# Kernel optimization log

Measured on AMD Instinct MI355X. Metric: run time of the kernel, lower is better.

## Reference

```python
import jax, jax.numpy as jnp
import numpy as np

IN_FEATURES = 4096
OUT_FEATURES = 8192
PADDED = 8192  # 2**ceil(log2(out_features))


def fwht(x):
    """Fast Walsh-Hadamard transform over last axis (n power of 2), normalized by 1/sqrt(n)."""
    orig_shape = x.shape
    n = orig_shape[-1]
    h = x.reshape(-1, n)
    step = 1
    while step < n:  # static loop, log2(n) iterations
        h = h.reshape(-1, n // (2 * step), 2, step)
        a = h[:, :, 0, :]
        b = h[:, :, 1, :]
        h = jnp.stack([a + b, a - b], axis=2).reshape(-1, n)
        step *= 2
    return (h * (1.0 / np.sqrt(n)).astype(np.float32)).reshape(orig_shape)


def setup_inputs() -> dict:
    key = jax.random.key(0)
    kx, kb, kg, kp = jax.random.split(key, 4)
    x = jax.random.normal(kx, (8192, IN_FEATURES), dtype=jnp.float32)
    B = jnp.where(jax.random.uniform(kb, (PADDED,)) < 0.5, -1.0, 1.0).astype(jnp.float32)
    G = jax.random.normal(kg, (PADDED,), dtype=jnp.float32)
    perm = jax.random.permutation(kp, PADDED).astype(jnp.int32)
    return {"x": x, "B": B, "G": G, "perm": perm}


def reference(x, B, G, perm):
    lead = x.shape[:-1]
    flat = x.reshape(-1, IN_FEATURES)
    pad_len = PADDED - IN_FEATURES
    if pad_len > 0:
        flat = jnp.pad(flat, ((0, 0), (0, pad_len)))
    out = flat * B[None, :]
    out = fwht(out)
    out = out[:, perm]
    out = out * G[None, :]
    out = fwht(out)
    out = out[:, :OUT_FEATURES]
    return out.reshape(*lead, OUT_FEATURES)
```

## Files before the change

### kernel.cpp

```cpp
#include <hip/hip_runtime.h>


constexpr int N  = 8192;
constexpr int NT = 256;
constexpr int NR = 32;
constexpr int LDS_WORDS = N + 2 * (N / 32);

__device__ __forceinline__ int padw(int w) { return w + 2 * (w >> 5); }

template <int FIRST_MASK>
__device__ __forceinline__ void butterfly(float v[NR]) {
    #pragma unroll
    for (int b = FIRST_MASK; b < NR; b <<= 1) {
        #pragma unroll
        for (int r = 0; r < NR; ++r) {
            if ((r & b) == 0) {
                float a = v[r], c = v[r ^ b];
                v[r]     = a + c;
                v[r ^ b] = a - c;
            }
        }
    }
}

__global__ __launch_bounds__(NT, 4) void fastfood_kernel(
    const float* __restrict__ x, const float* __restrict__ Bv,
    const float* __restrict__ Gv, const int* __restrict__ perm,
    float* __restrict__ out)
{
    __shared__ float lds[LDS_WORDS];
    const int t = threadIdx.x;
    const int row = blockIdx.x;
    const float* xrow = x + (size_t)row * 4096;

    const int wA = 2 * t;
    const int wB = t * 32;
    const int wC = (t >> 4) * 512 + (t & 15) * 2;

    float v[NR];

    #pragma unroll
    for (int m = 0; m < 8; ++m) {
        int j = m * 512 + wA;
        float2 xv = *(const float2*)(xrow + j);
        float2 bv = *(const float2*)(Bv + j);
        v[2 * m]     = xv.x * bv.x;
        v[2 * m + 1] = xv.y * bv.y;
    }
    #pragma unroll
    for (int m = 8; m < 16; ++m) { v[2 * m] = 0.f; v[2 * m + 1] = 0.f; }

    butterfly<1>(v);
    #pragma unroll
    for (int m = 0; m < 16; ++m)
        *(float2*)&lds[padw(m * 512 + wA)] = make_float2(v[2 * m], v[2 * m + 1]);
    __syncthreads();

    #pragma unroll
    for (int m = 0; m < 16; ++m) {
        float2 d = *(const float2*)&lds[padw(wB + 2 * m)];
        v[2 * m] = d.x; v[2 * m + 1] = d.y;
    }
    butterfly<2>(v);
    #pragma unroll
    for (int m = 0; m < 16; ++m)
        *(float2*)&lds[padw(wB + 2 * m)] = make_float2(v[2 * m], v[2 * m + 1]);
    __syncthreads();

    #pragma unroll
    for (int m = 0; m < 16; ++m) {
        float2 d = *(const float2*)&lds[padw(wC + m * 32)];
        v[2 * m] = d.x; v[2 * m + 1] = d.y;
    }
    int2 q[16];
    #pragma unroll
    for (int m = 0; m < 16; ++m)
        q[m] = *(const int2*)(perm + wC + m * 32);
    butterfly<2>(v);
    #pragma unroll
    for (int m = 0; m < 16; ++m)
        *(float2*)&lds[padw(wC + m * 32)] = make_float2(v[2 * m], v[2 * m + 1]);
    __syncthreads();

    #pragma unroll
    for (int m = 0; m < 16; ++m) {
        float2 g = *(const float2*)(Gv + wC + m * 32);
        v[2 * m]     = lds[q[m].x + 2 * (q[m].x >> 5)] * g.x;
        v[2 * m + 1] = lds[q[m].y + 2 * (q[m].y >> 5)] * g.y;
    }

    butterfly<1>(v);
    __syncthreads();
    #pragma unroll
    for (int m = 0; m < 16; ++m)
        *(float2*)&lds[padw(wC + m * 32)] = make_float2(v[2 * m], v[2 * m + 1]);
    __syncthreads();

    #pragma unroll
    for (int m = 0; m < 16; ++m) {
        float2 d = *(const float2*)&lds[padw(wB + 2 * m)];
        v[2 * m] = d.x; v[2 * m + 1] = d.y;
    }
    butterfly<2>(v);
    #pragma unroll
    for (int m = 0; m < 16; ++m)
        *(float2*)&lds[padw(wB + 2 * m)] = make_float2(v[2 * m], v[2 * m + 1]);
    __syncthreads();

    #pragma unroll
    for (int m = 0; m < 16; ++m) {
        float2 d = *(const float2*)&lds[padw(m * 512 + wA)];
        v[2 * m] = d.x; v[2 * m + 1] = d.y;
    }
    butterfly<2>(v);

    const float scale = 1.0f / 8192.0f;
    float* orow = out + (size_t)row * 8192;
    #pragma unroll
    for (int m = 0; m < 16; ++m) {
        int j = m * 512 + wA;
        *(float2*)(orow + j) = make_float2(v[2 * m] * scale, v[2 * m + 1] * scale);
    }
}

extern "C" void kernel_launch(void* const* d_in, const int* in_sizes, int n_in,
                              void* d_out, int out_size, void* d_ws, size_t ws_size,
                              hipStream_t stream) {
    const float* x    = (const float*)d_in[0];
    const float* Bv   = (const float*)d_in[1];
    const float* Gv   = (const float*)d_in[2];
    const int*   perm = (const int*)d_in[3];
    float* out = (float*)d_out;
    fastfood_kernel<<<dim3(8192), dim3(NT), 0, stream>>>(x, Bv, Gv, perm, out);
}
```

Measured before the change: 376.1 us.

## Use 512 threads with 16 registers per thread and four-pass FWHT staging

Doubles the block to 512 threads and halves the per-thread register array from 32 to 16 values, which adds an extra LDS exchange pass to each Walsh-Hadamard transform (four passes instead of three). New padded index mappings are introduced for each pass to avoid bank conflicts. The aim is more resident threads and lower register pressure to hide memory latency, at the cost of extra LDS traffic and additional barriers.

```diff
diff --git a/kernel.cpp b/kernel.cpp
--- a/kernel.cpp
+++ b/kernel.cpp
@@ -2,8 +2,8 @@
 
 
 constexpr int N  = 8192;
-constexpr int NT = 256;
-constexpr int NR = 32;
+constexpr int NT = 512;
+constexpr int NR = 16;
 constexpr int LDS_WORDS = N + 2 * (N / 32);
 
 __device__ __forceinline__ int padw(int w) { return w + 2 * (w >> 5); }
@@ -23,7 +23,7 @@
     }
 }
 
-__global__ __launch_bounds__(NT, 4) void fastfood_kernel(
+__global__ __launch_bounds__(NT, 8) void fastfood_kernel(
     const float* __restrict__ x, const float* __restrict__ Bv,
     const float* __restrict__ Gv, const int* __restrict__ perm,
     float* __restrict__ out)
@@ -34,57 +34,71 @@
     const float* xrow = x + (size_t)row * 4096;
 
     const int wA = 2 * t;
-    const int wB = t * 32;
-    const int wC = (t >> 4) * 512 + (t & 15) * 2;
+    const int pA = 2 * t + 2 * (t >> 4);
+    const int pB = 16 * t + 2 * (t >> 1);
+    const int wD = (t >> 6) * 1024 + (t & 63) * 2;
+    const int pD = (t >> 6) * 1088 + (t & 63) * 2 + 2 * ((t & 63) >> 4);
+    const int pC = (t >> 3) * 136 + (t & 7) * 2;
 
     float v[NR];
 
     #pragma unroll
-    for (int m = 0; m < 8; ++m) {
-        int j = m * 512 + wA;
+    for (int m = 0; m < 4; ++m) {
+        int j = m * 1024 + wA;
         float2 xv = *(const float2*)(xrow + j);
         float2 bv = *(const float2*)(Bv + j);
         v[2 * m]     = xv.x * bv.x;
         v[2 * m + 1] = xv.y * bv.y;
     }
     #pragma unroll
-    for (int m = 8; m < 16; ++m) { v[2 * m] = 0.f; v[2 * m + 1] = 0.f; }
+    for (int m = 4; m < 8; ++m) { v[2 * m] = 0.f; v[2 * m + 1] = 0.f; }
 
     butterfly<1>(v);
     #pragma unroll
-    for (int m = 0; m < 16; ++m)
-        *(float2*)&lds[padw(m * 512 + wA)] = make_float2(v[2 * m], v[2 * m + 1]);
+    for (int m = 0; m < 8; ++m)
+        *(float2*)&lds[pA + 1088 * m] = make_float2(v[2 * m], v[2 * m + 1]);
     __syncthreads();
 
     #pragma unroll
-    for (int m = 0; m < 16; ++m) {
-        float2 d = *(const float2*)&lds[padw(wB + 2 * m)];
+    for (int m = 0; m < 8; ++m) {
+        float2 d = *(const float2*)&lds[pB + 2 * m];
         v[2 * m] = d.x; v[2 * m + 1] = d.y;
     }
     butterfly<2>(v);
     #pragma unroll
-    for (int m = 0; m < 16; ++m)
-        *(float2*)&lds[padw(wB + 2 * m)] = make_float2(v[2 * m], v[2 * m + 1]);
+    for (int m = 0; m < 8; ++m)
+        *(float2*)&lds[pB + 2 * m] = make_float2(v[2 * m], v[2 * m + 1]);
     __syncthreads();
 
     #pragma unroll
-    for (int m = 0; m < 16; ++m) {
-        float2 d = *(const float2*)&lds[padw(wC + m * 32)];
+    for (int m = 0; m < 8; ++m) {
+        float2 d = *(const float2*)&lds[pC + 16 * m + 2 * (m >> 1)];
         v[2 * m] = d.x; v[2 * m + 1] = d.y;
     }
-    int2 q[16];
-    #pragma unroll
-    for (int m = 0; m < 16; ++m)
-        q[m] = *(const int2*)(perm + wC + m * 32);
     butterfly<2>(v);
     #pragma unroll
-    for (int m = 0; m < 16; ++m)
-        *(float2*)&lds[padw(wC + m * 32)] = make_float2(v[2 * m], v[2 * m + 1]);
+    for (int m = 0; m < 8; ++m)
+        *(float2*)&lds[pC + 16 * m + 2 * (m >> 1)] = make_float2(v[2 * m], v[2 * m + 1]);
     __syncthreads();
 
     #pragma unroll
-    for (int m = 0; m < 16; ++m) {
-        float2 g = *(const float2*)(Gv + wC + m * 32);
+    for (int m = 0; m < 8; ++m) {
+        float2 d = *(const float2*)&lds[pD + 136 * m];
+        v[2 * m] = d.x; v[2 * m + 1] = d.y;
+    }
+    int2 q[8];
+    #pragma unroll
+    for (int m = 0; m < 8; ++m)
+        q[m] = *(const int2*)(perm + wD + 128 * m);
+    butterfly<2>(v);
+    #pragma unroll
+    for (int m = 0; m < 8; ++m)
+        *(float2*)&lds[pD + 136 * m] = make_float2(v[2 * m], v[2 * m + 1]);
+    __syncthreads();
+
+    #pragma unroll
+    for (int m = 0; m < 8; ++m) {
+        float2 g = *(const float2*)(Gv + wD + 128 * m);
         v[2 * m]     = lds[q[m].x + 2 * (q[m].x >> 5)] * g.x;
         v[2 * m + 1] = lds[q[m].y + 2 * (q[m].y >> 5)] * g.y;
     }
@@ -92,24 +106,35 @@
     butterfly<1>(v);
     __syncthreads();
     #pragma unroll
-    for (int m = 0; m < 16; ++m)
-        *(float2*)&lds[padw(wC + m * 32)] = make_float2(v[2 * m], v[2 * m + 1]);
+    for (int m = 0; m < 8; ++m)
+        *(float2*)&lds[pD + 136 * m] = make_float2(v[2 * m], v[2 * m + 1]);
     __syncthreads();
 
     #pragma unroll
-    for (int m = 0; m < 16; ++m) {
-        float2 d = *(const float2*)&lds[padw(wB + 2 * m)];
+    for (int m = 0; m < 8; ++m) {
+        float2 d = *(const float2*)&lds[pC + 16 * m + 2 * (m >> 1)];
         v[2 * m] = d.x; v[2 * m + 1] = d.y;
     }
     butterfly<2>(v);
     #pragma unroll
-    for (int m = 0; m < 16; ++m)
-        *(float2*)&lds[padw(wB + 2 * m)] = make_float2(v[2 * m], v[2 * m + 1]);
+    for (int m = 0; m < 8; ++m)
+        *(float2*)&lds[pC + 16 * m + 2 * (m >> 1)] = make_float2(v[2 * m], v[2 * m + 1]);
     __syncthreads();
 
     #pragma unroll
-    for (int m = 0; m < 16; ++m) {
-        float2 d = *(const float2*)&lds[padw(m * 512 + wA)];
+    for (int m = 0; m < 8; ++m) {
+        float2 d = *(const float2*)&lds[pB + 2 * m];
+        v[2 * m] = d.x; v[2 * m + 1] = d.y;
+    }
+    butterfly<2>(v);
+    #pragma unroll
+    for (int m = 0; m < 8; ++m)
+        *(float2*)&lds[pB + 2 * m] = make_float2(v[2 * m], v[2 * m + 1]);
+    __syncthreads();
+
+    #pragma unroll
+    for (int m = 0; m < 8; ++m) {
+        float2 d = *(const float2*)&lds[pA + 1088 * m];
         v[2 * m] = d.x; v[2 * m + 1] = d.y;
     }
     butterfly<2>(v);
@@ -117,8 +142,8 @@
     const float scale = 1.0f / 8192.0f;
     float* orow = out + (size_t)row * 8192;
     #pragma unroll
-    for (int m = 0; m < 16; ++m) {
-        int j = m * 512 + wA;
+    for (int m = 0; m < 8; ++m) {
+        int j = m * 1024 + wA;
         *(float2*)(orow + j) = make_float2(v[2 * m] * scale, v[2 * m + 1] * scale);
     }
 }
```

New measurement: 373.8 us. No clear change (-0.6%).

## Exploit zero padding: compute first FWHT as 4096-point transform, reuse halves

Applied to the files above, without the earlier changes.

Because the upper half of the padded input is zero, the first 8192-point Walsh-Hadamard transform equals a 4096-point transform duplicated across both halves. The kernel now runs the first transform on 16 registers per thread over 4096 elements, using new LDS index layouts with precomputed padded offsets. The permuted gather masks indices with 4095 to read from the single half. This halves the butterfly arithmetic and LDS traffic of the first stage, at the cost of an extra sync stage and more intricate addressing.

```diff
diff --git a/kernel.cpp b/kernel.cpp
--- a/kernel.cpp
+++ b/kernel.cpp
@@ -1,19 +1,15 @@
 #include <hip/hip_runtime.h>
 
 
-constexpr int N  = 8192;
 constexpr int NT = 256;
-constexpr int NR = 32;
-constexpr int LDS_WORDS = N + 2 * (N / 32);
+constexpr int LDS_WORDS = 8192 + 2 * (8192 / 32);
 
-__device__ __forceinline__ int padw(int w) { return w + 2 * (w >> 5); }
-
-template <int FIRST_MASK>
-__device__ __forceinline__ void butterfly(float v[NR]) {
+template <int FIRST_MASK, int NREG>
+__device__ __forceinline__ void butterfly(float (&v)[NREG]) {
     #pragma unroll
-    for (int b = FIRST_MASK; b < NR; b <<= 1) {
+    for (int b = FIRST_MASK; b < NREG; b <<= 1) {
         #pragma unroll
-        for (int r = 0; r < NR; ++r) {
+        for (int r = 0; r < NREG; ++r) {
             if ((r & b) == 0) {
                 float a = v[r], c = v[r ^ b];
                 v[r]     = a + c;
@@ -33,92 +29,110 @@
     const int row = blockIdx.x;
     const float* xrow = x + (size_t)row * 4096;
 
-    const int wA = 2 * t;
-    const int wB = t * 32;
-    const int wC = (t >> 4) * 512 + (t & 15) * 2;
+    const int pA1 = 2 * t + 2 * (t >> 4);
+    const int pB1 = 16 * t + 2 * (t >> 1);
+    const int pC1 = 136 * (t >> 3) + 2 * (t & 7);
+    const int pD1 = 544 * (t >> 5) + 2 * (t & 31) + 2 * ((t & 31) >> 4);
+    const int wC2 = (t >> 4) * 512 + (t & 15) * 2;
+    const int pC2 = 544 * (t >> 4) + 2 * (t & 15);
+    const int pB2 = 34 * t;
+    const int wA2 = 2 * t;
+    const int pA2 = 2 * t + 2 * (t >> 4);
 
-    float v[NR];
+    float u[16];
 
     #pragma unroll
     for (int m = 0; m < 8; ++m) {
-        int j = m * 512 + wA;
+        int j = m * 512 + 2 * t;
         float2 xv = *(const float2*)(xrow + j);
         float2 bv = *(const float2*)(Bv + j);
-        v[2 * m]     = xv.x * bv.x;
-        v[2 * m + 1] = xv.y * bv.y;
+        u[2 * m]     = xv.x * bv.x;
+        u[2 * m + 1] = xv.y * bv.y;
     }
+
+    butterfly<1, 16>(u);
     #pragma unroll
-    for (int m = 8; m < 16; ++m) { v[2 * m] = 0.f; v[2 * m + 1] = 0.f; }
+    for (int m = 0; m < 8; ++m)
+        *(float2*)&lds[pA1 + 544 * m] = make_float2(u[2 * m], u[2 * m + 1]);
+    __syncthreads();
 
-    butterfly<1>(v);
+    #pragma unroll
+    for (int m = 0; m < 8; ++m) {
+        float2 d = *(const float2*)&lds[pB1 + 2 * m];
+        u[2 * m] = d.x; u[2 * m + 1] = d.y;
+    }
+    butterfly<2, 16>(u);
+    #pragma unroll
+    for (int m = 0; m < 8; ++m)
+        *(float2*)&lds[pB1 + 2 * m] = make_float2(u[2 * m], u[2 * m + 1]);
+    __syncthreads();
+
+    #pragma unroll
+    for (int m = 0; m < 8; ++m) {
+        float2 d = *(const float2*)&lds[pC1 + 16 * m + 2 * (m >> 1)];
+        u[2 * m] = d.x; u[2 * m + 1] = d.y;
+    }
+    butterfly<2, 16>(u);
+    #pragma unroll
+    for (int m = 0; m < 8; ++m)
+        *(float2*)&lds[pC1 + 16 * m + 2 * (m >> 1)] = make_float2(u[2 * m], u[2 * m + 1]);
+    __syncthreads();
+
+    #pragma unroll
+    for (int m = 0; m < 8; ++m) {
+        float2 d = *(const float2*)&lds[pD1 + 68 * m];
+        u[2 * m] = d.x; u[2 * m + 1] = d.y;
+    }
+    int2 q[16];
     #pragma unroll
     for (int m = 0; m < 16; ++m)
-        *(float2*)&lds[padw(m * 512 + wA)] = make_float2(v[2 * m], v[2 * m + 1]);
+        q[m] = *(const int2*)(perm + wC2 + 32 * m);
+    butterfly<4, 16>(u);
+    #pragma unroll
+    for (int m = 0; m < 8; ++m)
+        *(float2*)&lds[pD1 + 68 * m] = make_float2(u[2 * m], u[2 * m + 1]);
+    __syncthreads();
+
+    float v[32];
+    #pragma unroll
+    for (int m = 0; m < 16; ++m) {
+        float2 g = *(const float2*)(Gv + wC2 + 32 * m);
+        int wx = q[m].x & 4095;
+        int wy = q[m].y & 4095;
+        v[2 * m]     = lds[wx + 2 * (wx >> 5)] * g.x;
+        v[2 * m + 1] = lds[wy + 2 * (wy >> 5)] * g.y;
+    }
+
+    butterfly<1, 32>(v);
+    __syncthreads();
+    #pragma unroll
+    for (int m = 0; m < 16; ++m)
+        *(float2*)&lds[pC2 + 34 * m] = make_float2(v[2 * m], v[2 * m + 1]);
     __syncthreads();
 
     #pragma unroll
     for (int m = 0; m < 16; ++m) {
-        float2 d = *(const float2*)&lds[padw(wB + 2 * m)];
+        float2 d = *(const float2*)&lds[pB2 + 2 * m];
         v[2 * m] = d.x; v[2 * m + 1] = d.y;
     }
-    butterfly<2>(v);
+    butterfly<2, 32>(v);
     #pragma unroll
     for (int m = 0; m < 16; ++m)
-        *(float2*)&lds[padw(wB + 2 * m)] = make_float2(v[2 * m], v[2 * m + 1]);
+        *(float2*)&lds[pB2 + 2 * m] = make_float2(v[2 * m], v[2 * m + 1]);
     __syncthreads();
 
     #pragma unroll
     for (int m = 0; m < 16; ++m) {
-        float2 d = *(const float2*)&lds[padw(wC + m * 32)];
+        float2 d = *(const float2*)&lds[pA2 + 544 * m];
         v[2 * m] = d.x; v[2 * m + 1] = d.y;
     }
-    int2 q[16];
-    #pragma unroll
-    for (int m = 0; m < 16; ++m)
-        q[m] = *(const int2*)(perm + wC + m * 32);
-    butterfly<2>(v);
-    #pragma unroll
-    for (int m = 0; m < 16; ++m)
-        *(float2*)&lds[padw(wC + m * 32)] = make_float2(v[2 * m], v[2 * m + 1]);
-    __syncthreads();
-
-    #pragma unroll
-    for (int m = 0; m < 16; ++m) {
-        float2 g = *(const float2*)(Gv + wC + m * 32);
-        v[2 * m]     = lds[q[m].x + 2 * (q[m].x >> 5)] * g.x;
-        v[2 * m + 1] = lds[q[m].y + 2 * (q[m].y >> 5)] * g.y;
-    }
-
-    butterfly<1>(v);
-    __syncthreads();
-    #pragma unroll
-    for (int m = 0; m < 16; ++m)
-        *(float2*)&lds[padw(wC + m * 32)] = make_float2(v[2 * m], v[2 * m + 1]);
-    __syncthreads();
-
-    #pragma unroll
-    for (int m = 0; m < 16; ++m) {
-        float2 d = *(const float2*)&lds[padw(wB + 2 * m)];
-        v[2 * m] = d.x; v[2 * m + 1] = d.y;
-    }
-    butterfly<2>(v);
-    #pragma unroll
-    for (int m = 0; m < 16; ++m)
-        *(float2*)&lds[padw(wB + 2 * m)] = make_float2(v[2 * m], v[2 * m + 1]);
-    __syncthreads();
-
-    #pragma unroll
-    for (int m = 0; m < 16; ++m) {
-        float2 d = *(const float2*)&lds[padw(m * 512 + wA)];
-        v[2 * m] = d.x; v[2 * m + 1] = d.y;
-    }
-    butterfly<2>(v);
+    butterfly<2, 32>(v);
 
     const float scale = 1.0f / 8192.0f;
     float* orow = out + (size_t)row * 8192;
     #pragma unroll
     for (int m = 0; m < 16; ++m) {
-        int j = m * 512 + wA;
+        int j = m * 512 + wA2;
         *(float2*)(orow + j) = make_float2(v[2 * m] * scale, v[2 * m + 1] * scale);
     }
 }
```

Measured after the change: 374.6 us. About the same (-0.4%).
